# Performance work log

Measured on AMD Instinct MI355X. Metric: run time of the kernel, lower is better.

## Reference

```python
import jax, jax.numpy as jnp
import numpy as np

B, S, D, H, E, K = 4, 2048, 1024, 4096, 8, 2


def setup_inputs() -> dict:
    key = jax.random.key(0)
    ks = jax.random.split(key, 7)
    sd = 1.0 / np.sqrt(D)
    sh = 1.0 / np.sqrt(H)
    return {
        "x": jax.random.normal(ks[0], (B, S, D), dtype=jnp.float32),
        "Wg": jax.random.uniform(ks[1], (D, E), jnp.float32, -sd, sd),
        "bg": jnp.zeros((E,), jnp.float32),
        "W1": jax.random.uniform(ks[2], (E, D, H), jnp.float32, -sd, sd),
        "b1": jax.random.uniform(ks[3], (E, H), jnp.float32, -sd, sd),
        "W2": jax.random.uniform(ks[4], (E, H, D), jnp.float32, -sh, sh),
        "b2": jax.random.uniform(ks[5], (E, D), jnp.float32, -sh, sh),
    }


def reference(x, Wg, bg, W1, b1, W2, b2):
    # gating: softmax over experts, then top-k
    probs = jax.nn.softmax(x @ Wg + bg, axis=-1)            # [B,S,E]
    topv, topi = jax.lax.top_k(probs, K)                     # [B,S,K]
    # NOTE: original computes normalized scores but uses RAW top-k scores
    # scatter raw top-k scores back to dense per-expert weights [B,S,E]
    onehot = jax.nn.one_hot(topi, E, dtype=x.dtype)          # [B,S,K,E]
    w_dense = jnp.einsum("bske,bsk->bse", onehot, topv)      # [B,S,E]
    out = jnp.zeros_like(x)
    for e in range(E):
        h = jax.nn.relu(jnp.einsum("bsd,dh->bsh", x, W1[e]) + b1[e])
        y = jnp.einsum("bsh,hd->bsd", h, W2[e]) + b2[e]
        out = out + y * w_dense[..., e:e + 1]
    return out
```

## Files before the change

kernel.cpp:

```cpp
#include <hip/hip_runtime.h>

typedef unsigned short u16;
typedef __attribute__((ext_vector_type(8))) short bf16x8;
typedef __attribute__((ext_vector_type(8))) unsigned short u16x8;
typedef __attribute__((ext_vector_type(4))) float f32x4;

#define NTOK 8192
#define DDIM 1024
#define HDIM 4096
#define NEXP 8
#define NTILE 136

typedef __attribute__((address_space(1))) const void gvoid;
typedef __attribute__((address_space(3))) void lvoid;

__device__ __forceinline__ u16 f2b(float f) {
  unsigned u = __float_as_uint(f);
  u += 0x7fffu + ((u >> 16) & 1u);
  return (u16)(u >> 16);
}
__device__ __forceinline__ void glds16(const void* g, void* l) {
  __builtin_amdgcn_global_load_lds((gvoid*)g, (lvoid*)l, 16, 0, 0);
}

__global__ void convert_x_kernel(const float* __restrict__ src, u16* __restrict__ dst) {
  size_t i = ((size_t)blockIdx.x * 256 + threadIdx.x) * 8;
  float4 a = *(const float4*)(src + i);
  float4 b = *(const float4*)(src + i + 4);
  u16x8 o;
  o[0] = f2b(a.x); o[1] = f2b(a.y); o[2] = f2b(a.z); o[3] = f2b(a.w);
  o[4] = f2b(b.x); o[5] = f2b(b.y); o[6] = f2b(b.z); o[7] = f2b(b.w);
  *(u16x8*)(dst + i) = o;
}

__global__ void transpose_kernel(const float* __restrict__ src, u16* __restrict__ dst,
                                 int R, int C) {
  int e = blockIdx.z;
  src += (size_t)e * R * C;
  dst += (size_t)e * R * C;
  int r0 = blockIdx.y * 64, c0 = blockIdx.x * 64;
  __shared__ u16 T[64][68];
  int t = threadIdx.x;
  int rr = t >> 4, cc = (t & 15) * 4;
#pragma unroll
  for (int i = 0; i < 4; ++i) {
    int r = i * 16 + rr;
    float4 v = *(const float4*)(src + (size_t)(r0 + r) * C + c0 + cc);
    T[cc + 0][r] = f2b(v.x);
    T[cc + 1][r] = f2b(v.y);
    T[cc + 2][r] = f2b(v.z);
    T[cc + 3][r] = f2b(v.w);
  }
  __syncthreads();
#pragma unroll
  for (int i = 0; i < 4; ++i) {
    int c = i * 16 + rr;
    ushort4 o = *(const ushort4*)&T[c][cc];
    *(ushort4*)(dst + (size_t)(c0 + c) * R + r0 + cc) = o;
  }
}

__global__ void gate_kernel(const float* __restrict__ x, const float* __restrict__ Wg,
                            const float* __restrict__ bg, int* __restrict__ counts_pad,
                            int* __restrict__ pair_tok, float* __restrict__ pair_w,
                            int* __restrict__ tok_ep)
{
  int lane = threadIdx.x & 63;
  int wave = threadIdx.x >> 6;
  int tok = blockIdx.x * 4 + wave;
  const float* xr = x + (size_t)tok * DDIM + lane * 16;
  float acc[NEXP];
#pragma unroll
  for (int e = 0; e < NEXP; ++e) acc[e] = 0.f;
#pragma unroll
  for (int j = 0; j < 16; ++j) {
    float xf = xr[j];
    const float* wr = Wg + (size_t)(lane * 16 + j) * NEXP;
    float4 wa = *(const float4*)(wr);
    float4 wb = *(const float4*)(wr + 4);
    acc[0] = fmaf(xf, wa.x, acc[0]);
    acc[1] = fmaf(xf, wa.y, acc[1]);
    acc[2] = fmaf(xf, wa.z, acc[2]);
    acc[3] = fmaf(xf, wa.w, acc[3]);
    acc[4] = fmaf(xf, wb.x, acc[4]);
    acc[5] = fmaf(xf, wb.y, acc[5]);
    acc[6] = fmaf(xf, wb.z, acc[6]);
    acc[7] = fmaf(xf, wb.w, acc[7]);
  }
#pragma unroll
  for (int off = 32; off > 0; off >>= 1) {
#pragma unroll
    for (int e = 0; e < NEXP; ++e) acc[e] += __shfl_xor(acc[e], off, 64);
  }
  if (lane == 0) {
    float l[NEXP];
    float mx = -3.4e38f;
#pragma unroll
    for (int e = 0; e < NEXP; ++e) { l[e] = acc[e] + bg[e]; mx = fmaxf(mx, l[e]); }
    float s = 0.f;
#pragma unroll
    for (int e = 0; e < NEXP; ++e) { l[e] = __expf(l[e] - mx); s += l[e]; }
    float inv = 1.f / s;
    float v1 = -1.f; int i1 = 0;
#pragma unroll
    for (int e = 0; e < NEXP; ++e) { if (l[e] > v1) { v1 = l[e]; i1 = e; } }
    float v2 = -1.f; int i2 = 0;
#pragma unroll
    for (int e = 0; e < NEXP; ++e) { if (e != i1 && l[e] > v2) { v2 = l[e]; i2 = e; } }
    int p1 = atomicAdd(&counts_pad[i1 * 32], 1);
    pair_tok[i1 * NTOK + p1] = tok;
    pair_w[i1 * NTOK + p1] = v1 * inv;
    tok_ep[2 * tok + 0] = (i1 << 16) | p1;
    int p2 = atomicAdd(&counts_pad[i2 * 32], 1);
    pair_tok[i2 * NTOK + p2] = tok;
    pair_w[i2 * NTOK + p2] = v2 * inv;
    tok_ep[2 * tok + 1] = (i2 << 16) | p2;
  }
}

__global__ void offsets_kernel(const int* __restrict__ counts_pad, int* __restrict__ counts,
                               int* __restrict__ offsets, int* __restrict__ tile_e,
                               int* __restrict__ tile_i0, int* __restrict__ ntiles)
{
  if (threadIdx.x == 0) {
    int te[NTILE], ti[NTILE];
    int s = 0;
    for (int e = 0; e < NEXP; ++e) {
      int c = counts_pad[e * 32];
      counts[e] = c; offsets[e] = s; s += c;
    }
    int nt_ = 0;
    for (int e = 0; e < NEXP; ++e)
      for (int i0 = 0; i0 < counts[e]; i0 += 128) { te[nt_] = e; ti[nt_] = i0; nt_++; }
    for (int w = 0; w < NTILE; ++w) {
      int t = (w & 7) * 17 + (w >> 3);
      tile_e[w]  = (t < nt_) ? te[t] : -1;
      tile_i0[w] = (t < nt_) ? ti[t] : 0;
    }
    *ntiles = nt_;
  }
}

__device__ __forceinline__ void stage4(const u16* xa0, const u16* xa1,
                                       const u16* wb0, const u16* wb1,
                                       u16* Asb, u16* Bsb, int wave, int koff) {
  glds16(xa0 + koff, Asb + wave * 512);
  glds16(xa1 + koff, Asb + 2048 + wave * 512);
  glds16(wb0 + koff, Bsb + wave * 512);
  glds16(wb1 + koff, Bsb + 2048 + wave * 512);
}

__device__ __forceinline__ void mfma_tile(const u16* Asb, const u16* Bsb,
                                          f32x4 (&acc)[4][4],
                                          int wrr, int wc, int ln, int q) {
  bf16x8 af[4], bfr[4];
#pragma unroll
  for (int mt = 0; mt < 4; ++mt)
    af[mt] = *(const bf16x8*)(Asb + (wrr + mt * 16 + ln) * 32 + q * 8);
#pragma unroll
  for (int nt = 0; nt < 4; ++nt)
    bfr[nt] = *(const bf16x8*)(Bsb + (wc + nt * 16 + ln) * 32 + q * 8);
#pragma unroll
  for (int mt = 0; mt < 4; ++mt)
#pragma unroll
    for (int nt = 0; nt < 4; ++nt)
      acc[mt][nt] = __builtin_amdgcn_mfma_f32_16x16x32_bf16(af[mt], bfr[nt], acc[mt][nt], 0, 0, 0);
}

#define GEMM_LOOP(KDIM)                                                      \
  stage4(xa0, xa1, wb0, wb1, As[0], Bs[0], wave, 0);                         \
  stage4(xa0, xa1, wb0, wb1, As[1], Bs[1], wave, 32);                        \
  {                                                                          \
    int cur = 0, nx2 = 2;                                                    \
    for (int k0 = 0; k0 < (KDIM); k0 += 32) {                                \
      __builtin_amdgcn_sched_barrier(0);                                     \
      if (k0 + 32 < (KDIM))                                                  \
        asm volatile("s_waitcnt vmcnt(4) lgkmcnt(0)" ::: "memory");          \
      else                                                                   \
        asm volatile("s_waitcnt vmcnt(0) lgkmcnt(0)" ::: "memory");          \
      __builtin_amdgcn_s_barrier();                                          \
      __builtin_amdgcn_sched_barrier(0);                                     \
      if (k0 + 64 < (KDIM))                                                  \
        stage4(xa0, xa1, wb0, wb1, As[nx2], Bs[nx2], wave, k0 + 64);         \
      mfma_tile(As[cur], Bs[cur], acc, wrr, wc, ln, q);                      \
      cur = (cur == 2) ? 0 : cur + 1;                                        \
      nx2 = (nx2 == 2) ? 0 : nx2 + 1;                                        \
    }                                                                        \
  }

__global__ __launch_bounds__(256) void gemm1_kernel(
    const u16* __restrict__ xb, const u16* __restrict__ W1T,
    const float* __restrict__ b1, const int* __restrict__ counts,
    const int* __restrict__ offsets, const int* __restrict__ ntiles,
    const int* __restrict__ tile_e, const int* __restrict__ tile_i0,
    const int* __restrict__ pair_tok, u16* __restrict__ h, int hp, int p0)
{
  int bx = blockIdx.x;
  int e = tile_e[bx];
  if (e < 0) return;
  int i0 = tile_i0[bx];
  int cnt = counts[e];
  int n0 = blockIdx.y * 128;

  __shared__ __align__(16) u16 As[3][4096];
  __shared__ __align__(16) u16 Bs[3][4096];

  int t = threadIdx.x;
  int lane = t & 63;
  int wave = t >> 6;
  int rlim = cnt - i0;
  int rl = rlim - 1;

  const int* tokp = pair_tok + e * NTOK + i0;
  int arow = t >> 2;
  int c8 = (t & 3) * 8;
  const u16* xa0 = xb + (size_t)tokp[min(arow, rl)] * DDIM + c8;
  const u16* xa1 = xb + (size_t)tokp[min(arow + 64, rl)] * DDIM + c8;
  const u16* wb0 = W1T + (size_t)e * HDIM * DDIM + (size_t)(p0 + n0 + arow) * DDIM + c8;
  const u16* wb1 = wb0 + (size_t)64 * DDIM;

  f32x4 acc[4][4] = {};
  int wrr = (wave >> 1) * 64;
  int wc = (wave & 1) * 64;
  int ln = lane & 15;
  int q = lane >> 4;

  GEMM_LOOP(DDIM);

  int ob = offsets[e];
  float bb[4];
#pragma unroll
  for (int nt = 0; nt < 4; ++nt)
    bb[nt] = b1[(size_t)e * HDIM + p0 + n0 + wc + nt * 16 + ln];
  size_t hbase = (size_t)(ob + i0) * hp + n0 + wc;
#pragma unroll
  for (int mt = 0; mt < 4; ++mt) {
#pragma unroll
    for (int r = 0; r < 4; ++r) {
      int row = wrr + mt * 16 + q * 4 + r;
      if (row < rlim) {
        u16* hrow = h + hbase + (size_t)row * hp;
#pragma unroll
        for (int nt = 0; nt < 4; ++nt) {
          float v = acc[mt][nt][r] + bb[nt];
          hrow[nt * 16 + ln] = f2b(fmaxf(v, 0.f));
        }
      }
    }
  }
}

__global__ __launch_bounds__(256) void gemm2_kernel(
    const u16* __restrict__ h, const u16* __restrict__ W2T,
    const float* __restrict__ b2v, const int* __restrict__ counts,
    const int* __restrict__ offsets, const int* __restrict__ ntiles,
    const int* __restrict__ tile_e, const int* __restrict__ tile_i0,
    float* __restrict__ y, int hp, int p0, int first)
{
  int bx = blockIdx.x;
  int e = tile_e[bx];
  if (e < 0) return;
  int i0 = tile_i0[bx];
  int cnt = counts[e];
  int n0 = blockIdx.y * 128;

  __shared__ __align__(16) u16 As[3][4096];
  __shared__ __align__(16) u16 Bs[3][4096];

  int t = threadIdx.x;
  int lane = t & 63;
  int wave = t >> 6;
  int rlim = cnt - i0;
  int rl = rlim - 1;
  int rbase = offsets[e] + i0;

  int arow = t >> 2;
  int c8 = (t & 3) * 8;
  const u16* xa0 = h + (size_t)(rbase + min(arow, rl)) * hp + c8;
  const u16* xa1 = h + (size_t)(rbase + min(arow + 64, rl)) * hp + c8;
  const u16* wb0 = W2T + (size_t)e * DDIM * HDIM + (size_t)(n0 + arow) * HDIM + p0 + c8;
  const u16* wb1 = wb0 + (size_t)64 * HDIM;

  f32x4 acc[4][4] = {};
  int wrr = (wave >> 1) * 64;
  int wc = (wave & 1) * 64;
  int ln = lane & 15;
  int q = lane >> 4;

  GEMM_LOOP(hp);

  float bb[4];
#pragma unroll
  for (int nt = 0; nt < 4; ++nt)
    bb[nt] = first ? b2v[(size_t)e * DDIM + n0 + wc + nt * 16 + ln] : 0.f;
#pragma unroll
  for (int mt = 0; mt < 4; ++mt) {
#pragma unroll
    for (int r = 0; r < 4; ++r) {
      int row = wrr + mt * 16 + q * 4 + r;
      if (row < rlim) {
        float* yr = y + (size_t)(rbase + row) * DDIM + n0 + wc;
#pragma unroll
        for (int nt = 0; nt < 4; ++nt) {
          float v = acc[mt][nt][r] + bb[nt];
          if (first) yr[nt * 16 + ln] = v;
          else       yr[nt * 16 + ln] += v;
        }
      }
    }
  }
}

__global__ __launch_bounds__(256) void combine_kernel(
    const float* __restrict__ y, const int* __restrict__ tok_ep,
    const float* __restrict__ pair_w, const int* __restrict__ offsets,
    float* __restrict__ out)
{
  int tok = blockIdx.x;
  int ep1 = tok_ep[2 * tok + 0];
  int ep2 = tok_ep[2 * tok + 1];
  int e1 = ep1 >> 16, p1 = ep1 & 0xffff;
  int e2 = ep2 >> 16, p2 = ep2 & 0xffff;
  float w1 = pair_w[e1 * NTOK + p1];
  float w2 = pair_w[e2 * NTOK + p2];
  const float* r1 = y + (size_t)(offsets[e1] + p1) * DDIM;
  const float* r2 = y + (size_t)(offsets[e2] + p2) * DDIM;
  int c = threadIdx.x * 4;
  float4 a = *(const float4*)(r1 + c);
  float4 b = *(const float4*)(r2 + c);
  float4 o;
  o.x = w1 * a.x + w2 * b.x;
  o.y = w1 * a.y + w2 * b.y;
  o.z = w1 * a.z + w2 * b.z;
  o.w = w1 * a.w + w2 * b.w;
  *(float4*)(out + (size_t)tok * DDIM + c) = o;
}

extern "C" void kernel_launch(void* const* d_in, const int* in_sizes, int n_in,
                              void* d_out, int out_size, void* d_ws, size_t ws_size,
                              hipStream_t stream)
{
  const float* x  = (const float*)d_in[0];
  const float* Wg = (const float*)d_in[1];
  const float* bg = (const float*)d_in[2];
  const float* W1 = (const float*)d_in[3];
  const float* b1 = (const float*)d_in[4];
  const float* W2 = (const float*)d_in[5];
  const float* b2 = (const float*)d_in[6];
  float* out = (float*)d_out;

  char* ws = (char*)d_ws;
  int*   counts_pad = (int*)(ws + 0);
  int*   counts     = (int*)(ws + 1024);
  int*   offsets    = (int*)(ws + 1056);
  int*   ntiles     = (int*)(ws + 1088);
  int*   tile_e     = (int*)(ws + 1152);
  int*   tile_i0    = (int*)(ws + 2176);
  int*   tok_ep     = (int*)(ws + 4096);
  int*   pair_tok   = (int*)(ws + 69632);
  float* pair_w     = (float*)(ws + 331776);
  u16*   xb  = (u16*)(ws + 593920);
  u16*   W1T = (u16*)(ws + 593920 + 16777216);
  u16*   W2T = (u16*)(ws + 593920 + 16777216 + 67108864);
  float* yb  = (float*)(ws + 593920 + 16777216 + 2 * (size_t)67108864);
  u16*   hbuf = (u16*)(ws + 593920 + 16777216 + 3 * (size_t)67108864);
  size_t used_base = 593920 + 16777216 + 3 * (size_t)67108864;

  int hp = 256;
  const int cands[5] = {4096, 2048, 1024, 512, 256};
  for (int ci = 0; ci < 5; ++ci) {
    if (used_base + (size_t)16512 * cands[ci] * 2 <= ws_size) { hp = cands[ci]; break; }
  }

  hipMemsetAsync(counts_pad, 0, 1024, stream);
  convert_x_kernel<<<NTOK * DDIM / 2048, 256, 0, stream>>>(x, xb);
  transpose_kernel<<<dim3(HDIM / 64, DDIM / 64, NEXP), 256, 0, stream>>>(W1, W1T, DDIM, HDIM);
  transpose_kernel<<<dim3(DDIM / 64, HDIM / 64, NEXP), 256, 0, stream>>>(W2, W2T, HDIM, DDIM);
  gate_kernel<<<NTOK / 4, 256, 0, stream>>>(x, Wg, bg, counts_pad, pair_tok, pair_w, tok_ep);
  offsets_kernel<<<1, 64, 0, stream>>>(counts_pad, counts, offsets, tile_e, tile_i0, ntiles);
  for (int p0 = 0; p0 < HDIM; p0 += hp) {
    gemm1_kernel<<<dim3(NTILE, hp / 128), 256, 0, stream>>>(
        xb, W1T, b1, counts, offsets, ntiles, tile_e, tile_i0, pair_tok, hbuf, hp, p0);
    gemm2_kernel<<<dim3(NTILE, DDIM / 128), 256, 0, stream>>>(
        hbuf, W2T, b2, counts, offsets, ntiles, tile_e, tile_i0, yb, hp, p0, p0 == 0 ? 1 : 0);
  }
  combine_kernel<<<NTOK, 256, 0, stream>>>(yb, tok_ep, pair_w, offsets, out);
}
```

Before: 917.3 us.

## Fuse x bf16 conversion into gating and batch expert slot atomics per block

The separate fp32-to-bf16 conversion kernel is removed and the conversion is done inside the gate kernel, which already reads x, so x is read from memory once instead of twice. Each gate block now handles 64 tokens, counts expert slots with shared-memory atomics, and issues one global atomic per expert per block instead of one per token pair. The offsets kernel builds its tile table in parallel across threads instead of in a serial single-thread loop. Slot order within each expert changes, and the gate grid is much smaller, which lowers parallelism in that kernel.

```diff
diff --git a/kernel.cpp b/kernel.cpp
--- a/kernel.cpp
+++ b/kernel.cpp
@@ -10,6 +10,7 @@
 #define HDIM 4096
 #define NEXP 8
 #define NTILE 136
+#define GTOK 64
 
 typedef __attribute__((address_space(1))) const void gvoid;
 typedef __attribute__((address_space(3))) void lvoid;
@@ -21,16 +22,6 @@
 }
 __device__ __forceinline__ void glds16(const void* g, void* l) {
   __builtin_amdgcn_global_load_lds((gvoid*)g, (lvoid*)l, 16, 0, 0);
-}
-
-__global__ void convert_x_kernel(const float* __restrict__ src, u16* __restrict__ dst) {
-  size_t i = ((size_t)blockIdx.x * 256 + threadIdx.x) * 8;
-  float4 a = *(const float4*)(src + i);
-  float4 b = *(const float4*)(src + i + 4);
-  u16x8 o;
-  o[0] = f2b(a.x); o[1] = f2b(a.y); o[2] = f2b(a.z); o[3] = f2b(a.w);
-  o[4] = f2b(b.x); o[5] = f2b(b.y); o[6] = f2b(b.z); o[7] = f2b(b.w);
-  *(u16x8*)(dst + i) = o;
 }
 
 __global__ void transpose_kernel(const float* __restrict__ src, u16* __restrict__ dst,
@@ -60,61 +51,93 @@
   }
 }
 
-__global__ void gate_kernel(const float* __restrict__ x, const float* __restrict__ Wg,
-                            const float* __restrict__ bg, int* __restrict__ counts_pad,
-                            int* __restrict__ pair_tok, float* __restrict__ pair_w,
-                            int* __restrict__ tok_ep)
-{
-  int lane = threadIdx.x & 63;
-  int wave = threadIdx.x >> 6;
-  int tok = blockIdx.x * 4 + wave;
-  const float* xr = x + (size_t)tok * DDIM + lane * 16;
-  float acc[NEXP];
-#pragma unroll
-  for (int e = 0; e < NEXP; ++e) acc[e] = 0.f;
-#pragma unroll
-  for (int j = 0; j < 16; ++j) {
-    float xf = xr[j];
-    const float* wr = Wg + (size_t)(lane * 16 + j) * NEXP;
-    float4 wa = *(const float4*)(wr);
-    float4 wb = *(const float4*)(wr + 4);
-    acc[0] = fmaf(xf, wa.x, acc[0]);
-    acc[1] = fmaf(xf, wa.y, acc[1]);
-    acc[2] = fmaf(xf, wa.z, acc[2]);
-    acc[3] = fmaf(xf, wa.w, acc[3]);
-    acc[4] = fmaf(xf, wb.x, acc[4]);
-    acc[5] = fmaf(xf, wb.y, acc[5]);
-    acc[6] = fmaf(xf, wb.z, acc[6]);
-    acc[7] = fmaf(xf, wb.w, acc[7]);
-  }
-#pragma unroll
-  for (int off = 32; off > 0; off >>= 1) {
-#pragma unroll
-    for (int e = 0; e < NEXP; ++e) acc[e] += __shfl_xor(acc[e], off, 64);
-  }
-  if (lane == 0) {
-    float l[NEXP];
-    float mx = -3.4e38f;
-#pragma unroll
-    for (int e = 0; e < NEXP; ++e) { l[e] = acc[e] + bg[e]; mx = fmaxf(mx, l[e]); }
-    float s = 0.f;
-#pragma unroll
-    for (int e = 0; e < NEXP; ++e) { l[e] = __expf(l[e] - mx); s += l[e]; }
-    float inv = 1.f / s;
-    float v1 = -1.f; int i1 = 0;
-#pragma unroll
-    for (int e = 0; e < NEXP; ++e) { if (l[e] > v1) { v1 = l[e]; i1 = e; } }
-    float v2 = -1.f; int i2 = 0;
-#pragma unroll
-    for (int e = 0; e < NEXP; ++e) { if (e != i1 && l[e] > v2) { v2 = l[e]; i2 = e; } }
-    int p1 = atomicAdd(&counts_pad[i1 * 32], 1);
-    pair_tok[i1 * NTOK + p1] = tok;
-    pair_w[i1 * NTOK + p1] = v1 * inv;
-    tok_ep[2 * tok + 0] = (i1 << 16) | p1;
-    int p2 = atomicAdd(&counts_pad[i2 * 32], 1);
-    pair_tok[i2 * NTOK + p2] = tok;
-    pair_w[i2 * NTOK + p2] = v2 * inv;
-    tok_ep[2 * tok + 1] = (i2 << 16) | p2;
+__global__ __launch_bounds__(256) void gate_kernel(
+    const float* __restrict__ x, const float* __restrict__ Wg,
+    const float* __restrict__ bg, int* __restrict__ counts_pad,
+    int* __restrict__ pair_tok, float* __restrict__ pair_w,
+    int* __restrict__ tok_ep, u16* __restrict__ xb)
+{
+  __shared__ int lcnt[NEXP];
+  __shared__ int lbase[NEXP];
+  __shared__ u16 ent_e[GTOK * 2];
+  __shared__ u16 ent_pos[GTOK * 2];
+  __shared__ float ent_w[GTOK * 2];
+
+  int t = threadIdx.x;
+  if (t < NEXP) lcnt[t] = 0;
+  __syncthreads();
+
+  int lane = t & 63;
+  int wave = t >> 6;
+
+  for (int it = 0; it < 16; ++it) {
+    int ti = wave * 16 + it;
+    int tok = blockIdx.x * GTOK + ti;
+    const float* xr = x + (size_t)tok * DDIM + lane * 16;
+    float xv[16];
+#pragma unroll
+    for (int j = 0; j < 16; ++j) xv[j] = xr[j];
+    u16x8 o0, o1;
+#pragma unroll
+    for (int j = 0; j < 8; ++j) { o0[j] = f2b(xv[j]); o1[j] = f2b(xv[j + 8]); }
+    u16* xo = xb + (size_t)tok * DDIM + lane * 16;
+    *(u16x8*)(xo) = o0;
+    *(u16x8*)(xo + 8) = o1;
+
+    float acc[NEXP];
+#pragma unroll
+    for (int e = 0; e < NEXP; ++e) acc[e] = 0.f;
+#pragma unroll
+    for (int j = 0; j < 16; ++j) {
+      float xf = xv[j];
+      const float* wr = Wg + (size_t)(lane * 16 + j) * NEXP;
+      float4 wa = *(const float4*)(wr);
+      float4 wb = *(const float4*)(wr + 4);
+      acc[0] = fmaf(xf, wa.x, acc[0]);
+      acc[1] = fmaf(xf, wa.y, acc[1]);
+      acc[2] = fmaf(xf, wa.z, acc[2]);
+      acc[3] = fmaf(xf, wa.w, acc[3]);
+      acc[4] = fmaf(xf, wb.x, acc[4]);
+      acc[5] = fmaf(xf, wb.y, acc[5]);
+      acc[6] = fmaf(xf, wb.z, acc[6]);
+      acc[7] = fmaf(xf, wb.w, acc[7]);
+    }
+#pragma unroll
+    for (int off = 32; off > 0; off >>= 1) {
+#pragma unroll
+      for (int e = 0; e < NEXP; ++e) acc[e] += __shfl_xor(acc[e], off, 64);
+    }
+    if (lane == 0) {
+      float l[NEXP];
+      float mx = -3.4e38f;
+#pragma unroll
+      for (int e = 0; e < NEXP; ++e) { l[e] = acc[e] + bg[e]; mx = fmaxf(mx, l[e]); }
+      float s = 0.f;
+#pragma unroll
+      for (int e = 0; e < NEXP; ++e) { l[e] = __expf(l[e] - mx); s += l[e]; }
+      float inv = 1.f / s;
+      float v1 = -1.f; int i1 = 0;
+#pragma unroll
+      for (int e = 0; e < NEXP; ++e) { if (l[e] > v1) { v1 = l[e]; i1 = e; } }
+      float v2 = -1.f; int i2 = 0;
+#pragma unroll
+      for (int e = 0; e < NEXP; ++e) { if (e != i1 && l[e] > v2) { v2 = l[e]; i2 = e; } }
+      int p1 = atomicAdd(&lcnt[i1], 1);
+      ent_e[2 * ti] = (u16)i1; ent_pos[2 * ti] = (u16)p1; ent_w[2 * ti] = v1 * inv;
+      int p2 = atomicAdd(&lcnt[i2], 1);
+      ent_e[2 * ti + 1] = (u16)i2; ent_pos[2 * ti + 1] = (u16)p2; ent_w[2 * ti + 1] = v2 * inv;
+    }
+  }
+  __syncthreads();
+  if (t < NEXP) lbase[t] = atomicAdd(&counts_pad[t * 32], lcnt[t]);
+  __syncthreads();
+  if (t < GTOK * 2) {
+    int e = ent_e[t];
+    int p = lbase[e] + ent_pos[t];
+    int tok = blockIdx.x * GTOK + (t >> 1);
+    pair_tok[e * NTOK + p] = tok;
+    pair_w[e * NTOK + p] = ent_w[t];
+    tok_ep[2 * tok + (t & 1)] = (e << 16) | p;
   }
 }
 
@@ -122,22 +145,30 @@
                                int* __restrict__ offsets, int* __restrict__ tile_e,
                                int* __restrict__ tile_i0, int* __restrict__ ntiles)
 {
-  if (threadIdx.x == 0) {
-    int te[NTILE], ti[NTILE];
-    int s = 0;
+  __shared__ int cumt[NEXP + 1];
+  int t = threadIdx.x;
+  if (t == 0) {
+    int s = 0, ct = 0;
     for (int e = 0; e < NEXP; ++e) {
       int c = counts_pad[e * 32];
       counts[e] = c; offsets[e] = s; s += c;
-    }
-    int nt_ = 0;
-    for (int e = 0; e < NEXP; ++e)
-      for (int i0 = 0; i0 < counts[e]; i0 += 128) { te[nt_] = e; ti[nt_] = i0; nt_++; }
-    for (int w = 0; w < NTILE; ++w) {
-      int t = (w & 7) * 17 + (w >> 3);
-      tile_e[w]  = (t < nt_) ? te[t] : -1;
-      tile_i0[w] = (t < nt_) ? ti[t] : 0;
-    }
-    *ntiles = nt_;
+      cumt[e] = ct; ct += (c + 127) >> 7;
+    }
+    cumt[NEXP] = ct;
+    *ntiles = ct;
+  }
+  __syncthreads();
+  if (t < NTILE) {
+    int tt = (t & 7) * 17 + (t >> 3);
+    int ntot = cumt[NEXP];
+    int e = -1, i0 = 0;
+    if (tt < ntot) {
+#pragma unroll
+      for (int e2 = 0; e2 < NEXP; ++e2)
+        if (tt >= cumt[e2] && tt < cumt[e2 + 1]) { e = e2; i0 = (tt - cumt[e2]) << 7; }
+    }
+    tile_e[t] = e;
+    tile_i0[t] = i0;
   }
 }
 
@@ -373,11 +404,11 @@
   }
 
   hipMemsetAsync(counts_pad, 0, 1024, stream);
-  convert_x_kernel<<<NTOK * DDIM / 2048, 256, 0, stream>>>(x, xb);
   transpose_kernel<<<dim3(HDIM / 64, DDIM / 64, NEXP), 256, 0, stream>>>(W1, W1T, DDIM, HDIM);
   transpose_kernel<<<dim3(DDIM / 64, HDIM / 64, NEXP), 256, 0, stream>>>(W2, W2T, HDIM, DDIM);
-  gate_kernel<<<NTOK / 4, 256, 0, stream>>>(x, Wg, bg, counts_pad, pair_tok, pair_w, tok_ep);
-  offsets_kernel<<<1, 64, 0, stream>>>(counts_pad, counts, offsets, tile_e, tile_i0, ntiles);
+  gate_kernel<<<NTOK / GTOK, 256, 0, stream>>>(x, Wg, bg, counts_pad, pair_tok, pair_w,
+                                               tok_ep, xb);
+  offsets_kernel<<<1, 256, 0, stream>>>(counts_pad, counts, offsets, tile_e, tile_i0, ntiles);
   for (int p0 = 0; p0 < HDIM; p0 += hp) {
     gemm1_kernel<<<dim3(NTILE, hp / 128), 256, 0, stream>>>(
         xb, W1T, b1, counts, offsets, ntiles, tile_e, tile_i0, pair_tok, hbuf, hp, p0);
```

After: 800.2 us. -12.8%, faster.
